# Optimization experiments

Hardware: AMD Instinct MI355X
Metric: run time of the kernel (lower is better)

## Reference

```python
import jax, jax.numpy as jnp
import numpy as np

N = 10000      # nodes
E = 160000     # edges (avg degree 16)
D = 480        # node feat dim: 128x0e+64x1e+32x2e
SH = 9         # spherical harmonics dim, lmax=2, component norm
NB = 128       # radial basis count
H = 4          # attention heads
HD = D // H    # 120 = 32x0e+16x1o+8x2e
L = 6          # transformer blocks
G = 256        # graphs in batch
MID = 480      # ffn mid dim (irreps_mlp_mid)
S = 128        # scalar (0e) channels used by the output head
FCH = 64       # radial MLP hidden (fc_neurons)
CUTOFF = 5.0
AVG_DEG = 16.0
AVG_NODES = 18.0


def _sph_l2(vec):
    # real spherical harmonics l=0,1,2 on normalized vectors, 'component' normalization
    r = jnp.linalg.norm(vec, axis=-1, keepdims=True)
    u = vec / (r + 1e-9)
    x, y, z = u[..., 0], u[..., 1], u[..., 2]
    s3, s15, s5 = jnp.sqrt(3.0), jnp.sqrt(15.0), jnp.sqrt(5.0)
    return jnp.stack([
        jnp.ones_like(x),
        s3 * x, s3 * y, s3 * z,
        s15 * x * y, s15 * y * z, 0.5 * s5 * (3.0 * z * z - 1.0),
        s15 * x * z, 0.5 * s15 * (x * x - y * y)], axis=-1)


def _rbf(d):
    centers = jnp.linspace(0.0, CUTOFF, NB)
    w = CUTOFF / NB
    return jnp.exp(-0.5 * ((d[:, None] - centers) / w) ** 2)  # [E, NB]


def _ln(x):
    mu = jnp.mean(x, axis=-1, keepdims=True)
    var = jnp.var(x, axis=-1, keepdims=True)
    return (x - mu) * jax.lax.rsqrt(var + 1e-5)


def _radial_mlp(rb, w1, w2, w3):
    h = jax.nn.silu(rb @ w1)
    h = jax.nn.silu(h @ w2)
    return h @ w3


def _segment_softmax(logits, seg, num_segments):
    m = jax.ops.segment_max(logits, seg, num_segments=num_segments)
    ex = jnp.exp(logits - m[seg])
    s = jax.ops.segment_sum(ex, seg, num_segments=num_segments)
    return ex / (s[seg] + 1e-9)


def setup_inputs():
    key = jax.random.key(0)
    ks = jax.random.split(key, 24)
    def rn(k, shape, scale):
        return jax.random.normal(k, shape, dtype=jnp.float32) * scale
    return {
        'z': jax.random.randint(ks[0], (N,), 0, 100),
        'pos': jax.random.normal(ks[1], (N, 3), dtype=jnp.float32) * 3.0,
        'batch': jnp.sort(jax.random.randint(ks[2], (N,), 0, G)),
        'edge_src': jax.random.randint(ks[3], (E,), 0, N),
        'edge_dst': jax.random.randint(ks[4], (E,), 0, N),
        'atom_emb': rn(ks[5], (100, D), 1.0),
        'W_deg_sh': rn(ks[6], (SH, D), SH ** -0.5),
        'deg_w1': rn(ks[7], (NB, FCH), NB ** -0.5),
        'deg_w2': rn(ks[8], (FCH, FCH), FCH ** -0.5),
        'deg_w3': rn(ks[9], (FCH, D), FCH ** -0.5),
        'Wv': rn(ks[10], (L, D, D), D ** -0.5),
        'Wsh': rn(ks[11], (L, SH, D), SH ** -0.5),
        'rad_w1': rn(ks[12], (L, NB, FCH), NB ** -0.5),
        'rad_w2': rn(ks[13], (L, FCH, FCH), FCH ** -0.5),
        'rad_w3': rn(ks[14], (L, FCH, D), FCH ** -0.5),
        'attn_a': rn(ks[15], (L, H, HD), HD ** -0.5),
        'Wo': rn(ks[16], (L, D, D), D ** -0.5),
        'ffn_w1': rn(ks[17], (L, D, MID), D ** -0.5),
        'ffn_w2': rn(ks[18], (L, MID, D), MID ** -0.5),
        'head_w1': rn(ks[19], (S, S), S ** -0.5),
        'head_w2': rn(ks[20], (S, S), S ** -0.5),
    }


def reference(z, pos, batch, edge_src, edge_dst, atom_emb, W_deg_sh,
              deg_w1, deg_w2, deg_w3, Wv, Wsh, rad_w1, rad_w2, rad_w3,
              attn_a, Wo, ffn_w1, ffn_w2, head_w1, head_w2):
    # edge geometry features
    vec = pos[edge_src] - pos[edge_dst]                      # [E, 3]
    sh = _sph_l2(vec)                                        # [E, SH]
    rb = _rbf(jnp.linalg.norm(vec, axis=-1))                 # [E, NB]

    # node embedding + edge-degree embedding (scatter to dst, scaled by avg degree)
    emb = atom_emb[z]                                        # [N, D]
    deg_gate = _radial_mlp(rb, deg_w1, deg_w2, deg_w3)       # [E, D]
    deg = jax.ops.segment_sum((sh @ W_deg_sh) * deg_gate, edge_dst,
                              num_segments=N) / AVG_DEG
    x = emb + deg

    # equivariant tensor-product attention blocks (gather -> per-edge TP -> segment softmax -> scatter)
    for l in range(L):
        xn = _ln(x)
        v = xn[edge_src] @ Wv[l]                             # [E, D] gather + proj
        msg = v * (sh @ Wsh[l]) * _radial_mlp(rb, rad_w1[l], rad_w2[l], rad_w3[l])
        m = msg.reshape(E, H, HD)
        logits = jnp.einsum('ehd,hd->eh', jax.nn.leaky_relu(m, 0.2), attn_a[l])
        alpha = _segment_softmax(logits, edge_dst, N)        # [E, H]
        agg = jax.ops.segment_sum(m * alpha[:, :, None], edge_dst,
                                  num_segments=N).reshape(N, D)
        x = x + agg @ Wo[l]
        x = x + jax.nn.silu(_ln(x) @ ffn_w1[l]) @ ffn_w2[l]

    # output head on scalar channels, scaled scatter over molecules
    s = _ln(x[:, :S])
    h = jax.nn.silu(s @ head_w1) @ head_w2                   # [N, S]
    out = jax.ops.segment_sum(h, batch, num_segments=G) / jnp.sqrt(AVG_NODES)
    return out
```

## Files before the change

### kernel.cpp

```cpp
#include <hip/hip_runtime.h>
#include <hip/hip_bf16.h>
#include <math.h>

#define NN 10000
#define NE 160000
#define DIM 480
#define NSH 9
#define NBASIS 128
#define NHEAD 4
#define HDIM 120
#define NL 6
#define NG 256
#define NS 128
#define FCH 64
#define CUTOFF 5.0f

typedef __attribute__((ext_vector_type(8))) short bf8v;
typedef __attribute__((ext_vector_type(4))) float f4v;

__device__ __forceinline__ float silu_f(float v) { return v / (1.0f + __expf(-v)); }
__device__ __forceinline__ float bf2f(ushort u) { return __uint_as_float(((unsigned)u) << 16); }
__device__ __forceinline__ ushort f2bfu(float f) {
  __hip_bfloat16 h = __float2bfloat16(f);
  return *reinterpret_cast<ushort*>(&h);
}

__device__ __forceinline__ void nt_store16(char* dst, uint4 v) {
  unsigned* p = (unsigned*)dst;
  __builtin_nontemporal_store(v.x, p + 0);
  __builtin_nontemporal_store(v.y, p + 1);
  __builtin_nontemporal_store(v.z, p + 2);
  __builtin_nontemporal_store(v.w, p + 3);
}
__device__ __forceinline__ uint4 nt_load16(const char* src) {
  const unsigned* p = (const unsigned*)src;
  uint4 v;
  v.x = __builtin_nontemporal_load(p + 0);
  v.y = __builtin_nontemporal_load(p + 1);
  v.z = __builtin_nontemporal_load(p + 2);
  v.w = __builtin_nontemporal_load(p + 3);
  return v;
}

struct bf16x4 { __hip_bfloat16 v[4]; };

__global__ void k_zero_int(int* p, int n)
{
  int i = blockIdx.x * 256 + threadIdx.x;
  if (i < n) p[i] = 0;
}

__global__ void k_count(const int* __restrict__ edst, int* __restrict__ cnt)
{
  int e = blockIdx.x * 256 + threadIdx.x;
  if (e < NE) atomicAdd(&cnt[edst[e]], 1);
}

__global__ __launch_bounds__(1024)
void k_scan(const int* __restrict__ cnt, int* __restrict__ row_ptr)
{
  __shared__ int part[1024];
  int tid = threadIdx.x;
  const int per = 10;
  int base = tid * per;
  int s = 0;
  for (int i = 0; i < per; i++) { int idx = base + i; if (idx < NN) s += cnt[idx]; }
  part[tid] = s; __syncthreads();
  for (int off = 1; off < 1024; off <<= 1) {
    int v = (tid >= off) ? part[tid - off] : 0;
    __syncthreads();
    part[tid] += v;
    __syncthreads();
  }
  int run = (tid > 0) ? part[tid - 1] : 0;
  for (int i = 0; i < per; i++) {
    int idx = base + i;
    if (idx < NN) { row_ptr[idx] = run; run += cnt[idx]; }
  }
  if (tid == 1023) row_ptr[NN] = part[1023];
}

__global__ void k_fill(const int* __restrict__ edst, const int* __restrict__ row_ptr,
                       int* __restrict__ cursor, int* __restrict__ csr)
{
  int e = blockIdx.x * 256 + threadIdx.x;
  if (e >= NE) return;
  int d = edst[e];
  int p = atomicAdd(&cursor[d], 1);
  csr[row_ptr[d] + p] = e;
}

__global__ void k_geom_p(const float* __restrict__ pos, const int* __restrict__ esrc,
                         const int* __restrict__ edst, const int* __restrict__ csr,
                         __hip_bfloat16* __restrict__ shb, float* __restrict__ distp,
                         int* __restrict__ esrcp, int* __restrict__ edstp)
{
  int j = blockIdx.x * 256 + threadIdx.x;
  if (j >= NE) return;
  int e = csr[j];
  int s = esrc[e], d = edst[e];
  esrcp[j] = s;
  edstp[j] = d;
  float vx = pos[s*3+0] - pos[d*3+0];
  float vy = pos[s*3+1] - pos[d*3+1];
  float vz = pos[s*3+2] - pos[d*3+2];
  float r = sqrtf(vx*vx + vy*vy + vz*vz);
  distp[j] = r;
  float inv = 1.0f / (r + 1e-9f);
  float x = vx*inv, y = vy*inv, z = vz*inv;
  const float s3 = 1.7320508075688772f;
  const float s15 = 3.872983346207417f;
  const float s5 = 2.23606797749979f;
  float sv[9];
  sv[0] = 1.0f;
  sv[1] = s3*x; sv[2] = s3*y; sv[3] = s3*z;
  sv[4] = s15*x*y; sv[5] = s15*y*z; sv[6] = 0.5f*s5*(3.0f*z*z - 1.0f);
  sv[7] = s15*x*z; sv[8] = 0.5f*s15*(x*x - y*y);
  __hip_bfloat16* o = shb + (size_t)j * 16;
#pragma unroll
  for (int q = 0; q < 9; q++) o[q] = __float2bfloat16(sv[q]);
#pragma unroll
  for (int q = 9; q < 16; q++) o[q] = __float2bfloat16(0.f);
}

__global__ void k_prep(const float* __restrict__ deg_w3, const float* __restrict__ rad_w3,
                       const float* __restrict__ W_deg_sh, const float* __restrict__ Wsh,
                       __hip_bfloat16* __restrict__ w3T, __hip_bfloat16* __restrict__ wshT)
{
  int i = blockIdx.x * 256 + threadIdx.x;
  if (i < 7*512*64) {
    int l = i / (512*64); int r = i - l*512*64; int col = r >> 6; int k = r & 63;
    float v = 0.f;
    if (col < DIM) {
      const float* src = (l == 0) ? deg_w3 : rad_w3 + (size_t)(l-1)*FCH*DIM;
      v = src[k*DIM + col];
    }
    w3T[i] = __float2bfloat16(v);
  }
  int j = i - 7*512*64;
  if (j >= 0 && j < 7*512*32) {
    int l = j / (512*32); int r = j - l*512*32; int col = r >> 5; int q = r & 31;
    float v = 0.f;
    if (col < DIM && q < 9) {
      const float* src = (l == 0) ? W_deg_sh : Wsh + (size_t)(l-1)*NSH*DIM;
      v = src[q*DIM + col];
    }
    wshT[j] = __float2bfloat16(v);
  }
}

__global__ void k_prepw(const float* __restrict__ Wv, const float* __restrict__ Wo,
                        const float* __restrict__ f1, const float* __restrict__ f2,
                        const float* __restrict__ h1, const float* __restrict__ h2w,
                        __hip_bfloat16* __restrict__ WT)
{
  int i = blockIdx.x * 256 + threadIdx.x;
  const int big = 24*512*480;
  if (i < big) {
    int m = i / (512*480); int r = i - m*(512*480); int col = r / 480; int k = r - col*480;
    int l = m % 6; int t = m / 6;
    const float* src = (t==0 ? Wv : t==1 ? Wo : t==2 ? f1 : f2) + (size_t)l*DIM*DIM;
    float v = (col < DIM) ? src[k*DIM + col] : 0.f;
    WT[i] = __float2bfloat16(v);
  } else if (i < big + 2*128*128) {
    int j = i - big; int m = j / (128*128); int r = j - m*(128*128);
    int col = r >> 7; int k = r & 127;
    const float* src = m ? h2w : h1;
    WT[i] = __float2bfloat16(src[k*128 + col]);
  }
}

__global__ __launch_bounds__(256)
void k_radial(const float* __restrict__ dist, const float* __restrict__ w1,
              const float* __restrict__ w2, __hip_bfloat16* __restrict__ h2out)
{
  __shared__ float rbs[NBASIS][65];
  __shared__ float wsm[NBASIS * FCH];
  __shared__ float ds[64];
  int tid = threadIdx.x;
  int e0 = blockIdx.x * 64;
  if (tid < 64) ds[tid] = dist[e0 + tid];
  for (int i = tid; i < NBASIS * FCH; i += 256) wsm[i] = w1[i];
  __syncthreads();
  const float invw = (float)NBASIS / CUTOFF;
  for (int i = tid; i < NBASIS * 64; i += 256) {
    int k = i >> 6, e = i & 63;
    float c = k * (CUTOFF / 127.0f);
    float tt = (ds[e] - c) * invw;
    rbs[k][e] = __expf(-0.5f * tt * tt);
  }
  __syncthreads();
  int ty = tid >> 4, tx = tid & 15;
  float acc1[4][4] = {};
  for (int k = 0; k < NBASIS; k++) {
    float b[4];
#pragma unroll
    for (int j = 0; j < 4; j++) b[j] = wsm[k*FCH + tx*4 + j];
#pragma unroll
    for (int i = 0; i < 4; i++) {
      float a = rbs[k][ty*4 + i];
#pragma unroll
      for (int j = 0; j < 4; j++) acc1[i][j] = fmaf(a, b[j], acc1[i][j]);
    }
  }
  __syncthreads();
#pragma unroll
  for (int i = 0; i < 4; i++)
#pragma unroll
    for (int j = 0; j < 4; j++)
      rbs[tx*4 + j][ty*4 + i] = silu_f(acc1[i][j]);
  for (int i = tid; i < FCH * FCH; i += 256) wsm[i] = w2[i];
  __syncthreads();
  float acc2[4][4] = {};
  for (int k = 0; k < FCH; k++) {
    float b[4];
#pragma unroll
    for (int j = 0; j < 4; j++) b[j] = wsm[k*FCH + tx*4 + j];
#pragma unroll
    for (int i = 0; i < 4; i++) {
      float a = rbs[k][ty*4 + i];
#pragma unroll
      for (int j = 0; j < 4; j++) acc2[i][j] = fmaf(a, b[j], acc2[i][j]);
    }
  }
#pragma unroll
  for (int i = 0; i < 4; i++) {
    int e = e0 + ty*4 + i;
    bf16x4 p;
#pragma unroll
    for (int j = 0; j < 4; j++) p.v[j] = __float2bfloat16(silu_f(acc2[i][j]));
    *(bf16x4*)(h2out + (size_t)e*FCH + tx*4) = p;
  }
}

__global__ __launch_bounds__(256)
void k_stats(const float* __restrict__ in, float* __restrict__ st,
             int n, int cols, int stride)
{
  int row = blockIdx.x * 4 + (threadIdx.x >> 6);
  int lane = threadIdx.x & 63;
  if (row >= n) return;
  const float* r = in + (size_t)row * stride;
  float s = 0.f, ss = 0.f;
  for (int c = lane; c < cols; c += 64) { float v = r[c]; s += v; ss += v*v; }
  for (int off = 32; off > 0; off >>= 1) { s += __shfl_down(s, off); ss += __shfl_down(ss, off); }
  if (lane == 0) {
    float mu = s / cols;
    float var = ss / cols - mu * mu;
    st[row*2]   = mu;
    st[row*2+1] = rsqrtf(fmaxf(var, 0.f) + 1e-5f);
  }
}

template<int ADD, int SILU, int LNA, int OBF16>
__global__ __launch_bounds__(256)
void k_gemmm(const float* __restrict__ A, const __hip_bfloat16* __restrict__ BT,
             float* __restrict__ C, __hip_bfloat16* __restrict__ Cb,
             const float* __restrict__ st, int M, int K, int Nc, int lda)
{
  __shared__ __align__(16) char smA[4096];
  __shared__ __align__(16) char smB[8192];
  __shared__ float smu[64], srs[64];
  int tid = threadIdx.x;
  int lane = tid & 63;
  int wv = tid >> 6;
  int l15 = lane & 15, l4 = lane >> 4;
  int row0 = blockIdx.x * 64;
  int col0 = blockIdx.y * 128;
  if (LNA && tid < 64) {
    int gr = row0 + tid;
    float m2 = 0.f, r2 = 1.f;
    if (gr < M) { m2 = st[gr*2]; r2 = st[gr*2+1]; }
    smu[tid] = m2; srs[tid] = r2;
  }
  f4v z4 = {0.f,0.f,0.f,0.f};
  f4v acc[8];
#pragma unroll
  for (int ct = 0; ct < 8; ct++) acc[ct] = z4;

  int arow = tid >> 2, aq = tid & 3;
  int bcol = tid >> 1, bh = tid & 1;
  for (int k0 = 0; k0 < K; k0 += 32) {
    __syncthreads();
    {
      int grow = row0 + arow;
      float f[8];
      if (grow < M) {
        const float* ap = A + (size_t)grow * lda + k0 + aq*8;
        float4 v0 = *(const float4*)ap;
        float4 v1 = *(const float4*)(ap + 4);
        f[0]=v0.x; f[1]=v0.y; f[2]=v0.z; f[3]=v0.w;
        f[4]=v1.x; f[5]=v1.y; f[6]=v1.z; f[7]=v1.w;
      } else {
#pragma unroll
        for (int q = 0; q < 8; q++) f[q] = 0.f;
      }
      if (LNA) {
        float mu = smu[arow], rs = srs[arow];
#pragma unroll
        for (int q = 0; q < 8; q++) f[q] = (f[q] - mu) * rs;
      }
      unsigned u[4];
#pragma unroll
      for (int q = 0; q < 4; q++)
        u[q] = (unsigned)f2bfu(f[2*q]) | ((unsigned)f2bfu(f[2*q+1]) << 16);
      int base = arow*64 + aq*16;
      *(uint4*)(smA + (base ^ ((arow&7)<<4))) = make_uint4(u[0],u[1],u[2],u[3]);
    }
    {
      const ushort* bp = (const ushort*)BT + (size_t)(col0 + bcol) * K + k0 + bh*16;
      uint4 v0 = *(const uint4*)bp;
      uint4 v1 = *(const uint4*)(bp + 8);
      int base = bcol*64 + bh*32;
      *(uint4*)(smB + (base ^ ((bcol&7)<<4))) = v0;
      *(uint4*)(smB + ((base+16) ^ ((bcol&7)<<4))) = v1;
    }
    __syncthreads();
    int r0 = wv*16 + l15;
    bf8v a0 = *(const bf8v*)(smA + ((r0*64 + l4*16) ^ ((r0&7)<<4)));
#pragma unroll
    for (int ct = 0; ct < 8; ct++) {
      int cc = ct*16 + l15;
      bf8v b = *(const bf8v*)(smB + ((cc*64 + l4*16) ^ ((cc&7)<<4)));
      acc[ct] = __builtin_amdgcn_mfma_f32_16x16x32_bf16(a0, b, acc[ct], 0, 0, 0);
    }
  }
#pragma unroll
  for (int ct = 0; ct < 8; ct++)
#pragma unroll
  for (int e = 0; e < 4; e++) {
    int row = row0 + wv*16 + l4*4 + e;
    int col = col0 + ct*16 + l15;
    if (row < M && col < Nc) {
      float v = acc[ct][e];
      if (SILU) v = silu_f(v);
      if (OBF16) Cb[(size_t)row * Nc + col] = __float2bfloat16(v);
      else {
        float* p = C + (size_t)row * Nc + col;
        if (ADD) *p += v; else *p = v;
      }
    }
  }
}

template<int MODE, int STOREM>
__global__ __launch_bounds__(256)
void k_msgm(const __hip_bfloat16* __restrict__ h2, const __hip_bfloat16* __restrict__ shb,
            const int* __restrict__ esrcp, const int* __restrict__ edstp,
            const __hip_bfloat16* __restrict__ w3T, const __hip_bfloat16* __restrict__ wshT,
            const float* __restrict__ aa, const __hip_bfloat16* __restrict__ y,
            const float* __restrict__ alpha, float* __restrict__ outbuf,
            float* __restrict__ logitsP, __hip_bfloat16* __restrict__ msgb)
{
  __shared__ __align__(16) char sm_ab[24576];
  __shared__ __align__(16) char sm_sh[4096];
  __shared__ __align__(16) char sm_wsh[8192];
  __shared__ int srcs[(MODE<=1)?64:1];
  __shared__ int dsts[(MODE>=1)?64:1];
  __shared__ int segidL[(MODE>=1)?64:1];
  __shared__ int seg_dstL[(MODE>=1)?32:1];

  int bid = blockIdx.x;
  int swzb = (bid & 7) * 1250 + (bid >> 3);
  int e0   = (swzb >> 2) * 64;
  int col0 = (swzb & 3) * 128;
  int tid = threadIdx.x;
  int lane = tid & 63;
  int wv = tid >> 6;
  int l15 = lane & 15, l4 = lane >> 4;
  int wrow0 = wv * 16;

  for (int c = tid; c < 512; c += 256) {
    int r = c >> 3, s = c & 7;
    uint4 v = *(const uint4*)((const char*)h2 + (size_t)(e0 + r) * 128 + s * 16);
    *(uint4*)(sm_ab + ((r * 128 + s * 16) ^ ((r & 7) << 4))) = v;
  }
  for (int c = tid; c < 1024; c += 256) {
    int r = c >> 3, s = c & 7;
    uint4 v = *(const uint4*)((const char*)w3T + (size_t)(col0 + r) * 128 + s * 16);
    *(uint4*)(sm_ab + 8192 + ((r * 128 + s * 16) ^ ((r & 7) << 4))) = v;
  }
  {
    int r = tid >> 2, q = tid & 3;
    uint4 v = make_uint4(0u, 0u, 0u, 0u);
    if (q < 2)
      v = *(const uint4*)((const ushort*)shb + (size_t)(e0 + r) * 16 + q * 8);
    *(uint4*)(sm_sh + ((r * 64 + q * 16) ^ ((r & 7) << 4))) = v;
  }
  for (int c = tid; c < 512; c += 256) {
    int r = c >> 2, q = c & 3;
    uint4 v = *(const uint4*)((const ushort*)wshT + (size_t)(col0 + r) * 32 + q * 8);
    *(uint4*)(sm_wsh + ((r * 64 + q * 16) ^ ((r & 7) << 4))) = v;
  }
  if (tid < 64) {
    if (MODE <= 1) srcs[tid] = esrcp[e0 + tid];
    if (MODE >= 1) dsts[tid] = edstp[e0 + tid];
  }
  __syncthreads();

  int nseg = 0;
  if (MODE >= 1) {
    if (tid < 64) {
      bool flag = (tid == 0) || (dsts[tid] != dsts[tid - 1]);
      unsigned long long m = __ballot(flag ? 1 : 0);
      unsigned long long below = m & (~0ull >> (63 - tid));
      int sg = __popcll(below) - 1;
      segidL[tid] = sg;
      if (flag && sg < 32) seg_dstL[sg] = dsts[tid];
    }
    __syncthreads();
    nseg = segidL[63] + 1;
  }

  f4v z4 = {0.f, 0.f, 0.f, 0.f};
  f4v g[8];
#pragma unroll
  for (int ct = 0; ct < 8; ct++) g[ct] = z4;

#pragma unroll
  for (int ks = 0; ks < 2; ks++) {
    int k0b = (ks * 32 + l4 * 8) * 2;
    int r0 = wrow0 + l15;
    bf8v a0 = *(const bf8v*)(sm_ab + ((r0 * 128 + k0b) ^ ((r0 & 7) << 4)));
#pragma unroll
    for (int ct = 0; ct < 8; ct++) {
      int cc = ct * 16 + l15;
      bf8v b = *(const bf8v*)(sm_ab + 8192 + ((cc * 128 + k0b) ^ ((cc & 7) << 4)));
      g[ct] = __builtin_amdgcn_mfma_f32_16x16x32_bf16(a0, b, g[ct], 0, 0, 0);
    }
  }

  const ushort* yus = (const ushort*)y;
  int srcs4[4];
  float4 al4[4];
#pragma unroll
  for (int e = 0; e < 4; e++) {
    int rl = wrow0 + l4 * 4 + e;
    if (MODE <= 1) srcs4[e] = srcs[rl];
    if (MODE == 1) al4[e] = *(const float4*)(alpha + (size_t)(e0 + rl) * 4);
  }
  {
    int r0 = wrow0 + l15;
    bf8v shA = *(const bf8v*)(sm_sh + ((r0 * 64 + l4 * 16) ^ ((r0 & 7) << 4)));
#pragma unroll
    for (int ct = 0; ct < 8; ct++) {
      int cc = ct * 16 + l15;
      int col = col0 + cc;
      bf8v wB = *(const bf8v*)(sm_wsh + ((cc * 64 + l4 * 16) ^ ((cc & 7) << 4)));
      f4v sw4 = __builtin_amdgcn_mfma_f32_16x16x32_bf16(shA, wB, z4, 0, 0, 0);
#pragma unroll
      for (int e = 0; e < 4; e++) {
        float yv;
        if (MODE == 2) yv = 1.f;
        else yv = (col < DIM) ? bf2f(yus[(size_t)srcs4[e] * DIM + col]) : 0.f;
        float mv = yv * sw4[e] * g[ct][e];
        if (MODE == 1) {
          float av = (col < 120) ? al4[e].x : (col < 240) ? al4[e].y
                   : (col < 360) ? al4[e].z : al4[e].w;
          mv *= av;
        }
        if (MODE == 2) mv *= (1.0f / 16.0f);
        g[ct][e] = mv;
      }
    }
  }

  if (MODE == 0) {
    int hA = col0 / 120;
    float aav[8];
#pragma unroll
    for (int ct = 0; ct < 8; ct++) {
      int col = col0 + ct * 16 + l15;
      aav[ct] = (col < DIM) ? aa[col] : 0.f;
    }
#pragma unroll
    for (int e = 0; e < 4; e++) {
      float sA = 0.f, sB = 0.f;
#pragma unroll
      for (int ct = 0; ct < 8; ct++) {
        int col = col0 + ct * 16 + l15;
        float mv = g[ct][e];
        float lv = (mv > 0.f) ? mv : 0.2f * mv;
        float c = lv * aav[ct];
        if (col / 120 == hA) sA += c; else sB += c;
      }
#pragma unroll
      for (int off = 1; off < 16; off <<= 1) {
        sA += __shfl_xor(sA, off, 16);
        sB += __shfl_xor(sB, off, 16);
      }
      if (l15 == 0) {
        int row = e0 + wrow0 + l4 * 4 + e;
        logitsP[((size_t)row * NHEAD + hA) * 2] = sA;
        if (hA < 3) logitsP[((size_t)row * NHEAD + hA + 1) * 2 + 1] = sB;
      }
    }
    if (STOREM) {
      __syncthreads();
#pragma unroll
      for (int ct = 0; ct < 8; ct++) {
        int cc = ct * 16 + l15;
        int ebase = wrow0 + l4 * 4;
        ushort4 pk;
        pk.x = f2bfu(g[ct][0]); pk.y = f2bfu(g[ct][1]);
        pk.z = f2bfu(g[ct][2]); pk.w = f2bfu(g[ct][3]);
        *(ushort4*)(sm_ab + ((cc * 128 + ebase * 2) ^ ((cc & 7) << 4))) = pk;
      }
      __syncthreads();
      char* gdst = (char*)msgb + (size_t)swzb * 16384;
#pragma unroll
      for (int k = 0; k < 4; k++) {
        int o = tid * 16 + k * 4096;
        uint4 v = *(const uint4*)(sm_ab + o);
        nt_store16(gdst + o, v);
      }
    }
    return;
  }

  if (nseg > 32) {
#pragma unroll
    for (int e = 0; e < 4; e++) {
      int rl = wrow0 + l4 * 4 + e;
      int dd = dsts[rl];
#pragma unroll
      for (int ct = 0; ct < 8; ct++) {
        int col = col0 + ct * 16 + l15;
        if (col < DIM) atomicAdd(&outbuf[(size_t)dd * DIM + col], g[ct][e]);
      }
    }
    return;
  }

  __syncthreads();
#pragma unroll
  for (int ct = 0; ct < 8; ct++) {
    int cc = ct * 16 + l15;
    int ebase = wrow0 + l4 * 4;
    ushort4 pk;
    pk.x = f2bfu(g[ct][0]); pk.y = f2bfu(g[ct][1]);
    pk.z = f2bfu(g[ct][2]); pk.w = f2bfu(g[ct][3]);
    *(ushort4*)(sm_ab + ((cc * 128 + ebase * 2) ^ ((cc & 7) << 4))) = pk;
  }
  __syncthreads();

  f4v p[2][2];
  p[0][0] = z4; p[0][1] = z4; p[1][0] = z4; p[1][1] = z4;
#pragma unroll
  for (int ks = 0; ks < 2; ks++) {
    int k0 = ks * 32 + l4 * 8;
    bf8v a0, a1;
#pragma unroll
    for (int e2 = 0; e2 < 8; e2++) {
      int sg = segidL[k0 + e2];
      a0[e2] = (sg == l15)      ? (short)0x3F80 : (short)0;
      a1[e2] = (sg == l15 + 16) ? (short)0x3F80 : (short)0;
    }
#pragma unroll
    for (int c2 = 0; c2 < 2; c2++) {
      int cc = (wv * 2 + c2) * 16 + l15;
      bf8v bm = *(const bf8v*)(sm_ab + ((cc * 128 + k0 * 2) ^ ((cc & 7) << 4)));
      p[0][c2] = __builtin_amdgcn_mfma_f32_16x16x32_bf16(a0, bm, p[0][c2], 0, 0, 0);
      p[1][c2] = __builtin_amdgcn_mfma_f32_16x16x32_bf16(a1, bm, p[1][c2], 0, 0, 0);
    }
  }
#pragma unroll
  for (int rt = 0; rt < 2; rt++)
#pragma unroll
  for (int c2 = 0; c2 < 2; c2++)
#pragma unroll
  for (int e = 0; e < 4; e++) {
    int seg = rt * 16 + l4 * 4 + e;
    int col = col0 + (wv * 2 + c2) * 16 + l15;
    if (seg < nseg && col < DIM) {
      float v = p[rt][c2][e];
      float* ptr = outbuf + (size_t)seg_dstL[seg] * DIM + col;
      if (seg == 0 || seg == nseg - 1) atomicAdd(ptr, v);
      else if (MODE == 1) *ptr = v;
      else *ptr += v;
    }
  }
}

__global__ __launch_bounds__(256)
void k_aggm(const __hip_bfloat16* __restrict__ msgb, const int* __restrict__ edstp,
            const float* __restrict__ alpha, float* __restrict__ agg)
{
  __shared__ __align__(16) char smM[16384];
  __shared__ __align__(16) float alsq[64][4];
  __shared__ int dsts[64];
  __shared__ int segidL[64];
  __shared__ int seg_dstL[32];

  int bid = blockIdx.x;
  int swzb = (bid & 7) * 1250 + (bid >> 3);
  int e0   = (swzb >> 2) * 64;
  int col0 = (swzb & 3) * 128;
  int tid = threadIdx.x;
  int lane = tid & 63;
  int wv = tid >> 6;
  int l15 = lane & 15, l4 = lane >> 4;

  if (tid < 64) {
    dsts[tid] = edstp[e0 + tid];
    *(float4*)&alsq[tid][0] = *(const float4*)(alpha + (size_t)(e0 + tid) * 4);
  }
  __syncthreads();

  int nseg = 0;
  if (tid < 64) {
    bool flag = (tid == 0) || (dsts[tid] != dsts[tid - 1]);
    unsigned long long m = __ballot(flag ? 1 : 0);
    unsigned long long below = m & (~0ull >> (63 - tid));
    int sg = __popcll(below) - 1;
    segidL[tid] = sg;
    if (flag && sg < 32) seg_dstL[sg] = dsts[tid];
  }
  __syncthreads();
  nseg = segidL[63] + 1;

  const char* gsrc = (const char*)msgb + (size_t)swzb * 16384;
  uint4 vv[4];
#pragma unroll
  for (int k = 0; k < 4; k++) {
    int o = tid * 16 + k * 4096;
    uint4 v = nt_load16(gsrc + o);
    int cc = o >> 7;
    int col = col0 + cc;
    int h = (col < DIM) ? (col / 120) : 3;
    int be = ((o & 127) ^ ((cc & 7) << 4)) >> 1;
    unsigned w[4] = {v.x, v.y, v.z, v.w};
#pragma unroll
    for (int q = 0; q < 4; q++) {
      float lo = bf2f((ushort)(w[q] & 0xffffu)) * alsq[be + 2*q][h];
      float hi = bf2f((ushort)(w[q] >> 16))     * alsq[be + 2*q + 1][h];
      w[q] = (unsigned)f2bfu(lo) | ((unsigned)f2bfu(hi) << 16);
    }
    vv[k] = make_uint4(w[0], w[1], w[2], w[3]);
    *(uint4*)(smM + o) = vv[k];
  }
  __syncthreads();

  if (nseg > 32) {
#pragma unroll
    for (int k = 0; k < 4; k++) {
      int o = tid * 16 + k * 4096;
      int cc = o >> 7;
      int col = col0 + cc;
      if (col >= DIM) continue;
      int be = ((o & 127) ^ ((cc & 7) << 4)) >> 1;
      unsigned w[4] = {vv[k].x, vv[k].y, vv[k].z, vv[k].w};
#pragma unroll
      for (int q = 0; q < 4; q++) {
        atomicAdd(&agg[(size_t)dsts[be + 2*q]   * DIM + col], bf2f((ushort)(w[q] & 0xffffu)));
        atomicAdd(&agg[(size_t)dsts[be + 2*q+1] * DIM + col], bf2f((ushort)(w[q] >> 16)));
      }
    }
    return;
  }

  f4v z4 = {0.f,0.f,0.f,0.f};
  f4v p[2][2];
  p[0][0] = z4; p[0][1] = z4; p[1][0] = z4; p[1][1] = z4;
#pragma unroll
  for (int ks = 0; ks < 2; ks++) {
    int k0 = ks * 32 + l4 * 8;
    bf8v a0, a1;
#pragma unroll
    for (int e2 = 0; e2 < 8; e2++) {
      int sg = segidL[k0 + e2];
      a0[e2] = (sg == l15)      ? (short)0x3F80 : (short)0;
      a1[e2] = (sg == l15 + 16) ? (short)0x3F80 : (short)0;
    }
#pragma unroll
    for (int c2 = 0; c2 < 2; c2++) {
      int cc = (wv * 2 + c2) * 16 + l15;
      bf8v bm = *(const bf8v*)(smM + ((cc * 128 + k0 * 2) ^ ((cc & 7) << 4)));
      p[0][c2] = __builtin_amdgcn_mfma_f32_16x16x32_bf16(a0, bm, p[0][c2], 0, 0, 0);
      p[1][c2] = __builtin_amdgcn_mfma_f32_16x16x32_bf16(a1, bm, p[1][c2], 0, 0, 0);
    }
  }
#pragma unroll
  for (int rt = 0; rt < 2; rt++)
#pragma unroll
  for (int c2 = 0; c2 < 2; c2++)
#pragma unroll
  for (int e = 0; e < 4; e++) {
    int seg = rt * 16 + l4 * 4 + e;
    int col = col0 + (wv * 2 + c2) * 16 + l15;
    if (seg < nseg && col < DIM) {
      float v = p[rt][c2][e];
      float* ptr = agg + (size_t)seg_dstL[seg] * DIM + col;
      if (seg == 0 || seg == nseg - 1) atomicAdd(ptr, v);
      else *ptr = v;
    }
  }
}

__global__ void k_alpha(const int* __restrict__ row_ptr, const float* __restrict__ logitsP,
                        float* __restrict__ alpha)
{
  int i = blockIdx.x * 256 + threadIdx.x;
  if (i >= NN * NHEAD) return;
  int d = i >> 2, h = i & 3;
  int beg = row_ptr[d], end = row_ptr[d+1];
  if (beg == end) return;
  float m = -1e30f;
  for (int j = beg; j < end; j++) {
    float L = logitsP[((size_t)j*NHEAD + h)*2] + logitsP[((size_t)j*NHEAD + h)*2 + 1];
    m = fmaxf(m, L);
  }
  float s = 0.f;
  for (int j = beg; j < end; j++) {
    float L = logitsP[((size_t)j*NHEAD + h)*2] + logitsP[((size_t)j*NHEAD + h)*2 + 1];
    float ex = __expf(L - m);
    alpha[(size_t)j*NHEAD + h] = ex;
    s += ex;
  }
  float inv = 1.f / (s + 1e-9f);
  for (int j = beg; j < end; j++) alpha[(size_t)j*NHEAD + h] *= inv;
}

__global__ void k_init_x(const int* __restrict__ z, const float* __restrict__ emb,
                         float* __restrict__ x)
{
  int i = blockIdx.x * 256 + threadIdx.x;
  if (i >= NN * DIM) return;
  int n = i / DIM, c = i - n * DIM;
  x[i] = emb[(size_t)z[n]*DIM + c];
}

__global__ void k_scatter(const float* __restrict__ h, const int* __restrict__ batch,
                          float* __restrict__ out)
{
  int i = blockIdx.x * 256 + threadIdx.x;
  if (i >= NN * NS) return;
  int n = i >> 7;
  atomicAdd(&out[(size_t)batch[n]*NS + (i & 127)], h[i] * 0.23570226039551584f);
}

extern "C" void kernel_launch(void* const* d_in, const int* in_sizes, int n_in,
                              void* d_out, int out_size, void* d_ws, size_t ws_size,
                              hipStream_t stream)
{
  const int*   z        = (const int*)  d_in[0];
  const float* pos      = (const float*)d_in[1];
  const int*   batch    = (const int*)  d_in[2];
  const int*   esrc     = (const int*)  d_in[3];
  const int*   edst     = (const int*)  d_in[4];
  const float* atom_emb = (const float*)d_in[5];
  const float* W_deg_sh = (const float*)d_in[6];
  const float* deg_w1   = (const float*)d_in[7];
  const float* deg_w2   = (const float*)d_in[8];
  const float* deg_w3   = (const float*)d_in[9];
  const float* Wv       = (const float*)d_in[10];
  const float* Wsh      = (const float*)d_in[11];
  const float* rad_w1   = (const float*)d_in[12];
  const float* rad_w2   = (const float*)d_in[13];
  const float* rad_w3   = (const float*)d_in[14];
  const float* attn_a   = (const float*)d_in[15];
  const float* Wo       = (const float*)d_in[16];
  const float* ffn_w1   = (const float*)d_in[17];
  const float* ffn_w2   = (const float*)d_in[18];
  const float* head_w1  = (const float*)d_in[19];
  const float* head_w2  = (const float*)d_in[20];
  float* out = (float*)d_out;

  float* x      = (float*)d_ws;
  float* statsb = x      + (size_t)NN * DIM;
  float* agg    = statsb + (size_t)NN * 2;
  float* distp  = agg    + (size_t)NN * DIM;
  float* logitsP= distp  + (size_t)NE;
  float* alphab = logitsP+ (size_t)NE * NHEAD * 2;
  __hip_bfloat16* yb    = (__hip_bfloat16*)(alphab + (size_t)NE * NHEAD);
  __hip_bfloat16* h2b   = yb + (size_t)NN * DIM;
  __hip_bfloat16* shb16 = h2b + (size_t)NE * FCH;
  __hip_bfloat16* w3Tb  = shb16 + (size_t)NE * 16;
  __hip_bfloat16* wshTb = w3Tb + (size_t)7 * 512 * 64;
  __hip_bfloat16* bigWT = wshTb + (size_t)7 * 512 * 32;
  int* cnt      = (int*)(bigWT + (size_t)24*512*480 + 2*128*128);
  int* row_ptr  = cnt + NN;
  int* csr      = row_ptr + NN + 1;
  int* cursor   = csr + NE;
  int* esrcp    = cursor + NN;
  int* edstp    = esrcp + NE;
  __hip_bfloat16* msgb = (__hip_bfloat16*)(edstp + NE);
  float* tmp = logitsP;

  size_t needed = (size_t)((char*)msgb + (size_t)10000 * 16384 - (char*)d_ws);
  bool fast = ws_size >= needed;

  dim3 b256(256);
  k_zero_int<<<(NN+255)/256, b256, 0, stream>>>(cnt, NN);
  k_count<<<(NE+255)/256, b256, 0, stream>>>(edst, cnt);
  k_scan<<<1, 1024, 0, stream>>>(cnt, row_ptr);
  k_zero_int<<<(NN+255)/256, b256, 0, stream>>>(cursor, NN);
  k_fill<<<(NE+255)/256, b256, 0, stream>>>(edst, row_ptr, cursor, csr);
  k_geom_p<<<(NE+255)/256, b256, 0, stream>>>(pos, esrc, edst, csr, shb16, distp, esrcp, edstp);
  k_prep<<<(7*512*64 + 7*512*32 + 255)/256, b256, 0, stream>>>(deg_w3, rad_w3, W_deg_sh, Wsh,
      w3Tb, wshTb);
  k_prepw<<<(24*512*480 + 2*128*128 + 255)/256, b256, 0, stream>>>(Wv, Wo, ffn_w1, ffn_w2,
      head_w1, head_w2, bigWT);
  hipMemsetAsync(logitsP, 0, (size_t)NE * NHEAD * 2 * sizeof(float), stream);

  k_radial<<<NE/64, b256, 0, stream>>>(distp, deg_w1, deg_w2, h2b);
  k_init_x<<<(NN*DIM+255)/256, b256, 0, stream>>>(z, atom_emb, x);
  k_msgm<2,0><<<10000, b256, 0, stream>>>(h2b, shb16, esrcp, edstp, w3Tb, wshTb,
      nullptr, nullptr, nullptr, x, nullptr, nullptr);

  dim3 gemm_grid(157, 4);
  dim3 head_grid(157, 1);
  for (int l = 0; l < NL; l++) {
    const float* w1_l  = rad_w1 + (size_t)l*NBASIS*FCH;
    const float* w2_l  = rad_w2 + (size_t)l*FCH*FCH;
    const float* aa_l  = attn_a + (size_t)l*NHEAD*HDIM;
    const __hip_bfloat16* w3T_l  = w3Tb  + (size_t)(l+1)*512*64;
    const __hip_bfloat16* wshT_l = wshTb + (size_t)(l+1)*512*32;
    const __hip_bfloat16* WvT_l = bigWT + (size_t)(0+l)*512*480;
    const __hip_bfloat16* WoT_l = bigWT + (size_t)(6+l)*512*480;
    const __hip_bfloat16* F1T_l = bigWT + (size_t)(12+l)*512*480;
    const __hip_bfloat16* F2T_l = bigWT + (size_t)(18+l)*512*480;

    k_stats<<<(NN+3)/4, b256, 0, stream>>>(x, statsb, NN, DIM, DIM);
    k_gemmm<0,0,1,1><<<gemm_grid, b256, 0, stream>>>(x, WvT_l, nullptr, yb, statsb,
        NN, DIM, DIM, DIM);
    k_radial<<<NE/64, b256, 0, stream>>>(distp, w1_l, w2_l, h2b);
    if (fast) {
      k_msgm<0,1><<<10000, b256, 0, stream>>>(h2b, shb16, esrcp, edstp, w3T_l, wshT_l,
          aa_l, yb, nullptr, nullptr, logitsP, msgb);
      k_alpha<<<(NN*NHEAD+255)/256, b256, 0, stream>>>(row_ptr, logitsP, alphab);
      hipMemsetAsync(agg, 0, (size_t)NN * DIM * sizeof(float), stream);
      k_aggm<<<10000, b256, 0, stream>>>(msgb, edstp, alphab, agg);
    } else {
      k_msgm<0,0><<<10000, b256, 0, stream>>>(h2b, shb16, esrcp, edstp, w3T_l, wshT_l,
          aa_l, yb, nullptr, nullptr, logitsP, nullptr);
      k_alpha<<<(NN*NHEAD+255)/256, b256, 0, stream>>>(row_ptr, logitsP, alphab);
      hipMemsetAsync(agg, 0, (size_t)NN * DIM * sizeof(float), stream);
      k_msgm<1,0><<<10000, b256, 0, stream>>>(h2b, shb16, esrcp, edstp, w3T_l, wshT_l,
          nullptr, yb, alphab, agg, nullptr, nullptr);
    }
    k_gemmm<1,0,0,0><<<gemm_grid, b256, 0, stream>>>(agg, WoT_l, x, nullptr, nullptr,
        NN, DIM, DIM, DIM);
    k_stats<<<(NN+3)/4, b256, 0, stream>>>(x, statsb, NN, DIM, DIM);
    k_gemmm<0,1,1,0><<<gemm_grid, b256, 0, stream>>>(x, F1T_l, agg, nullptr, statsb,
        NN, DIM, DIM, DIM);
    k_gemmm<1,0,0,0><<<gemm_grid, b256, 0, stream>>>(agg, F2T_l, x, nullptr, nullptr,
        NN, DIM, DIM, DIM);
  }

  const __hip_bfloat16* H1T = bigWT + (size_t)24*512*480;
  const __hip_bfloat16* H2T = H1T + 128*128;
  k_stats<<<(NN+3)/4, b256, 0, stream>>>(x, statsb, NN, NS, DIM);
  k_gemmm<0,1,1,0><<<head_grid, b256, 0, stream>>>(x, H1T, agg, nullptr, statsb,
      NN, NS, NS, DIM);
  k_gemmm<0,0,0,0><<<head_grid, b256, 0, stream>>>(agg, H2T, tmp, nullptr, nullptr,
      NN, NS, NS, NS);
  hipMemsetAsync(d_out, 0, (size_t)NG * NS * sizeof(float), stream);
  k_scatter<<<(NN*NS+255)/256, b256, 0, stream>>>(tmp, batch, out);
}
```

Baseline: 2.570 ms.

## Loop over all column tiles inside each msgm block and accumulate full logits

Each k_msgm block now handles 64 edges across all four 128-column tiles in an internal loop, instead of launching one block per (edge block, column tile). The per-edge h2 and sh tiles are loaded once and reused across tiles, and the head logits are summed in registers, so the partial-logit buffer, its memset and the two-part sum in k_alpha go away. The cost is four times fewer blocks (2500 instead of 10000) doing more serial work each, with extra syncs and per-tile weight reloads, so latency hiding may suffer.

```diff
diff --git a/kernel.cpp b/kernel.cpp
--- a/kernel.cpp
+++ b/kernel.cpp
@@ -14,6 +14,7 @@
 #define NS 128
 #define FCH 64
 #define CUTOFF 5.0f
+#define NEB 2500
 
 typedef __attribute__((ext_vector_type(8))) short bf8v;
 typedef __attribute__((ext_vector_type(4))) float f4v;
@@ -350,9 +351,10 @@
             const __hip_bfloat16* __restrict__ w3T, const __hip_bfloat16* __restrict__ wshT,
             const float* __restrict__ aa, const __hip_bfloat16* __restrict__ y,
             const float* __restrict__ alpha, float* __restrict__ outbuf,
-            float* __restrict__ logitsP, __hip_bfloat16* __restrict__ msgb)
-{
-  __shared__ __align__(16) char sm_ab[24576];
+            float* __restrict__ logits, __hip_bfloat16* __restrict__ msgb)
+{
+  __shared__ __align__(16) char sm_h2[8192];
+  __shared__ __align__(16) char sm_w3[16384];
   __shared__ __align__(16) char sm_sh[4096];
   __shared__ __align__(16) char sm_wsh[8192];
   __shared__ int srcs[(MODE<=1)?64:1];
@@ -361,9 +363,12 @@
   __shared__ int seg_dstL[(MODE>=1)?32:1];
 
   int bid = blockIdx.x;
-  int swzb = (bid & 7) * 1250 + (bid >> 3);
-  int e0   = (swzb >> 2) * 64;
-  int col0 = (swzb & 3) * 128;
+  int xcd = bid & 7;
+  const int qq = NEB >> 3, rr = NEB & 7;
+  int basee = (xcd < rr) ? xcd * (qq + 1) : rr * (qq + 1) + (xcd - rr) * qq;
+  int eblk = basee + (bid >> 3);
+  int e0 = eblk * 64;
+
   int tid = threadIdx.x;
   int lane = tid & 63;
   int wv = tid >> 6;
@@ -373,12 +378,7 @@
   for (int c = tid; c < 512; c += 256) {
     int r = c >> 3, s = c & 7;
     uint4 v = *(const uint4*)((const char*)h2 + (size_t)(e0 + r) * 128 + s * 16);
-    *(uint4*)(sm_ab + ((r * 128 + s * 16) ^ ((r & 7) << 4))) = v;
-  }
-  for (int c = tid; c < 1024; c += 256) {
-    int r = c >> 3, s = c & 7;
-    uint4 v = *(const uint4*)((const char*)w3T + (size_t)(col0 + r) * 128 + s * 16);
-    *(uint4*)(sm_ab + 8192 + ((r * 128 + s * 16) ^ ((r & 7) << 4))) = v;
+    *(uint4*)(sm_h2 + ((r * 128 + s * 16) ^ ((r & 7) << 4))) = v;
   }
   {
     int r = tid >> 2, q = tid & 3;
@@ -386,11 +386,6 @@
     if (q < 2)
       v = *(const uint4*)((const ushort*)shb + (size_t)(e0 + r) * 16 + q * 8);
     *(uint4*)(sm_sh + ((r * 64 + q * 16) ^ ((r & 7) << 4))) = v;
-  }
-  for (int c = tid; c < 512; c += 256) {
-    int r = c >> 2, q = c & 3;
-    uint4 v = *(const uint4*)((const ushort*)wshT + (size_t)(col0 + r) * 32 + q * 8);
-    *(uint4*)(sm_wsh + ((r * 64 + q * 16) ^ ((r & 7) << 4))) = v;
   }
   if (tid < 64) {
     if (MODE <= 1) srcs[tid] = esrcp[e0 + tid];
@@ -412,25 +407,6 @@
     nseg = segidL[63] + 1;
   }
 
-  f4v z4 = {0.f, 0.f, 0.f, 0.f};
-  f4v g[8];
-#pragma unroll
-  for (int ct = 0; ct < 8; ct++) g[ct] = z4;
-
-#pragma unroll
-  for (int ks = 0; ks < 2; ks++) {
-    int k0b = (ks * 32 + l4 * 8) * 2;
-    int r0 = wrow0 + l15;
-    bf8v a0 = *(const bf8v*)(sm_ab + ((r0 * 128 + k0b) ^ ((r0 & 7) << 4)));
-#pragma unroll
-    for (int ct = 0; ct < 8; ct++) {
-      int cc = ct * 16 + l15;
-      bf8v b = *(const bf8v*)(sm_ab + 8192 + ((cc * 128 + k0b) ^ ((cc & 7) << 4)));
-      g[ct] = __builtin_amdgcn_mfma_f32_16x16x32_bf16(a0, b, g[ct], 0, 0, 0);
-    }
-  }
-
-  const ushort* yus = (const ushort*)y;
   int srcs4[4];
   float4 al4[4];
 #pragma unroll
@@ -439,63 +415,134 @@
     if (MODE <= 1) srcs4[e] = srcs[rl];
     if (MODE == 1) al4[e] = *(const float4*)(alpha + (size_t)(e0 + rl) * 4);
   }
-  {
-    int r0 = wrow0 + l15;
-    bf8v shA = *(const bf8v*)(sm_sh + ((r0 * 64 + l4 * 16) ^ ((r0 & 7) << 4)));
-#pragma unroll
-    for (int ct = 0; ct < 8; ct++) {
-      int cc = ct * 16 + l15;
-      int col = col0 + cc;
-      bf8v wB = *(const bf8v*)(sm_wsh + ((cc * 64 + l4 * 16) ^ ((cc & 7) << 4)));
-      f4v sw4 = __builtin_amdgcn_mfma_f32_16x16x32_bf16(shA, wB, z4, 0, 0, 0);
-#pragma unroll
-      for (int e = 0; e < 4; e++) {
-        float yv;
-        if (MODE == 2) yv = 1.f;
-        else yv = (col < DIM) ? bf2f(yus[(size_t)srcs4[e] * DIM + col]) : 0.f;
-        float mv = yv * sw4[e] * g[ct][e];
-        if (MODE == 1) {
-          float av = (col < 120) ? al4[e].x : (col < 240) ? al4[e].y
-                   : (col < 360) ? al4[e].z : al4[e].w;
-          mv *= av;
+
+  const ushort* yus = (const ushort*)y;
+  f4v z4 = {0.f, 0.f, 0.f, 0.f};
+  float lacc[4][4];
+  if (MODE == 0) {
+#pragma unroll
+    for (int e = 0; e < 4; e++)
+#pragma unroll
+      for (int h = 0; h < 4; h++) lacc[e][h] = 0.f;
+  }
+
+#pragma unroll
+  for (int ci = 0; ci < 4; ci++) {
+    int col0 = ci * 128;
+    __syncthreads();
+    for (int c = tid; c < 1024; c += 256) {
+      int r = c >> 3, s = c & 7;
+      uint4 v = *(const uint4*)((const char*)w3T + (size_t)(col0 + r) * 128 + s * 16);
+      *(uint4*)(sm_w3 + ((r * 128 + s * 16) ^ ((r & 7) << 4))) = v;
+    }
+    for (int c = tid; c < 512; c += 256) {
+      int r = c >> 2, q = c & 3;
+      uint4 v = *(const uint4*)((const ushort*)wshT + (size_t)(col0 + r) * 32 + q * 8);
+      *(uint4*)(sm_wsh + ((r * 64 + q * 16) ^ ((r & 7) << 4))) = v;
+    }
+    __syncthreads();
+
+    f4v g[8];
+#pragma unroll
+    for (int ct = 0; ct < 8; ct++) g[ct] = z4;
+
+#pragma unroll
+    for (int ks = 0; ks < 2; ks++) {
+      int k0b = (ks * 32 + l4 * 8) * 2;
+      int r0 = wrow0 + l15;
+      bf8v a0 = *(const bf8v*)(sm_h2 + ((r0 * 128 + k0b) ^ ((r0 & 7) << 4)));
+#pragma unroll
+      for (int ct = 0; ct < 8; ct++) {
+        int cc = ct * 16 + l15;
+        bf8v b = *(const bf8v*)(sm_w3 + ((cc * 128 + k0b) ^ ((cc & 7) << 4)));
+        g[ct] = __builtin_amdgcn_mfma_f32_16x16x32_bf16(a0, b, g[ct], 0, 0, 0);
+      }
+    }
+
+    {
+      int r0 = wrow0 + l15;
+      bf8v shA = *(const bf8v*)(sm_sh + ((r0 * 64 + l4 * 16) ^ ((r0 & 7) << 4)));
+#pragma unroll
+      for (int ct = 0; ct < 8; ct++) {
+        int cc = ct * 16 + l15;
+        int col = col0 + cc;
+        bf8v wB = *(const bf8v*)(sm_wsh + ((cc * 64 + l4 * 16) ^ ((cc & 7) << 4)));
+        f4v sw4 = __builtin_amdgcn_mfma_f32_16x16x32_bf16(shA, wB, z4, 0, 0, 0);
+#pragma unroll
+        for (int e = 0; e < 4; e++) {
+          float yv;
+          if (MODE == 2) yv = 1.f;
+          else yv = (col < DIM) ? bf2f(yus[(size_t)srcs4[e] * DIM + col]) : 0.f;
+          float mv = yv * sw4[e] * g[ct][e];
+          if (MODE == 1) {
+            float av = (col < 120) ? al4[e].x : (col < 240) ? al4[e].y
+                     : (col < 360) ? al4[e].z : al4[e].w;
+            mv *= av;
+          }
+          if (MODE == 2) mv *= (1.0f / 16.0f);
+          g[ct][e] = mv;
         }
-        if (MODE == 2) mv *= (1.0f / 16.0f);
-        g[ct][e] = mv;
-      }
-    }
-  }
-
-  if (MODE == 0) {
-    int hA = col0 / 120;
-    float aav[8];
-#pragma unroll
-    for (int ct = 0; ct < 8; ct++) {
-      int col = col0 + ct * 16 + l15;
-      aav[ct] = (col < DIM) ? aa[col] : 0.f;
-    }
-#pragma unroll
-    for (int e = 0; e < 4; e++) {
-      float sA = 0.f, sB = 0.f;
+      }
+    }
+
+    if (MODE == 0) {
+      float aav[8];
 #pragma unroll
       for (int ct = 0; ct < 8; ct++) {
         int col = col0 + ct * 16 + l15;
-        float mv = g[ct][e];
-        float lv = (mv > 0.f) ? mv : 0.2f * mv;
-        float c = lv * aav[ct];
-        if (col / 120 == hA) sA += c; else sB += c;
-      }
-#pragma unroll
-      for (int off = 1; off < 16; off <<= 1) {
-        sA += __shfl_xor(sA, off, 16);
-        sB += __shfl_xor(sB, off, 16);
-      }
-      if (l15 == 0) {
-        int row = e0 + wrow0 + l4 * 4 + e;
-        logitsP[((size_t)row * NHEAD + hA) * 2] = sA;
-        if (hA < 3) logitsP[((size_t)row * NHEAD + hA + 1) * 2 + 1] = sB;
-      }
-    }
-    if (STOREM) {
+        aav[ct] = (col < DIM) ? aa[col] : 0.f;
+      }
+#pragma unroll
+      for (int e = 0; e < 4; e++) {
+        float sA = 0.f, sB = 0.f;
+#pragma unroll
+        for (int ct = 0; ct < 8; ct++) {
+          int col = col0 + ct * 16 + l15;
+          float mv = g[ct][e];
+          float lv = (mv > 0.f) ? mv : 0.2f * mv;
+          float c = lv * aav[ct];
+          if (col / 120 == ci) sA += c; else sB += c;
+        }
+#pragma unroll
+        for (int off = 1; off < 16; off <<= 1) {
+          sA += __shfl_xor(sA, off, 16);
+          sB += __shfl_xor(sB, off, 16);
+        }
+        lacc[e][ci] += sA;
+        if (ci < 3) lacc[e][ci + 1] += sB;
+      }
+      if (STOREM) {
+        __syncthreads();
+#pragma unroll
+        for (int ct = 0; ct < 8; ct++) {
+          int cc = ct * 16 + l15;
+          int ebase = wrow0 + l4 * 4;
+          ushort4 pk;
+          pk.x = f2bfu(g[ct][0]); pk.y = f2bfu(g[ct][1]);
+          pk.z = f2bfu(g[ct][2]); pk.w = f2bfu(g[ct][3]);
+          *(ushort4*)(sm_w3 + ((cc * 128 + ebase * 2) ^ ((cc & 7) << 4))) = pk;
+        }
+        __syncthreads();
+        char* gdst = (char*)msgb + (size_t)(eblk * 4 + ci) * 16384;
+#pragma unroll
+        for (int k = 0; k < 4; k++) {
+          int o = tid * 16 + k * 4096;
+          uint4 v = *(const uint4*)(sm_w3 + o);
+          nt_store16(gdst + o, v);
+        }
+      }
+    } else if (nseg > 32) {
+#pragma unroll
+      for (int e = 0; e < 4; e++) {
+        int rl = wrow0 + l4 * 4 + e;
+        int dd = dsts[rl];
+#pragma unroll
+        for (int ct = 0; ct < 8; ct++) {
+          int col = col0 + ct * 16 + l15;
+          if (col < DIM) atomicAdd(&outbuf[(size_t)dd * DIM + col], g[ct][e]);
+        }
+      }
+    } else {
       __syncthreads();
 #pragma unroll
       for (int ct = 0; ct < 8; ct++) {
@@ -504,80 +551,58 @@
         ushort4 pk;
         pk.x = f2bfu(g[ct][0]); pk.y = f2bfu(g[ct][1]);
         pk.z = f2bfu(g[ct][2]); pk.w = f2bfu(g[ct][3]);
-        *(ushort4*)(sm_ab + ((cc * 128 + ebase * 2) ^ ((cc & 7) << 4))) = pk;
+        *(ushort4*)(sm_w3 + ((cc * 128 + ebase * 2) ^ ((cc & 7) << 4))) = pk;
       }
       __syncthreads();
-      char* gdst = (char*)msgb + (size_t)swzb * 16384;
-#pragma unroll
-      for (int k = 0; k < 4; k++) {
-        int o = tid * 16 + k * 4096;
-        uint4 v = *(const uint4*)(sm_ab + o);
-        nt_store16(gdst + o, v);
-      }
-    }
-    return;
-  }
-
-  if (nseg > 32) {
+      f4v p[2][2];
+      p[0][0] = z4; p[0][1] = z4; p[1][0] = z4; p[1][1] = z4;
+#pragma unroll
+      for (int ks = 0; ks < 2; ks++) {
+        int k0 = ks * 32 + l4 * 8;
+        bf8v a0, a1;
+#pragma unroll
+        for (int e2 = 0; e2 < 8; e2++) {
+          int sg = segidL[k0 + e2];
+          a0[e2] = (sg == l15)      ? (short)0x3F80 : (short)0;
+          a1[e2] = (sg == l15 + 16) ? (short)0x3F80 : (short)0;
+        }
+#pragma unroll
+        for (int c2 = 0; c2 < 2; c2++) {
+          int cc = (wv * 2 + c2) * 16 + l15;
+          bf8v bm = *(const bf8v*)(sm_w3 + ((cc * 128 + k0 * 2) ^ ((cc & 7) << 4)));
+          p[0][c2] = __builtin_amdgcn_mfma_f32_16x16x32_bf16(a0, bm, p[0][c2], 0, 0, 0);
+          p[1][c2] = __builtin_amdgcn_mfma_f32_16x16x32_bf16(a1, bm, p[1][c2], 0, 0, 0);
+        }
+      }
+#pragma unroll
+      for (int rt = 0; rt < 2; rt++)
+#pragma unroll
+      for (int c2 = 0; c2 < 2; c2++)
+#pragma unroll
+      for (int e = 0; e < 4; e++) {
+        int seg = rt * 16 + l4 * 4 + e;
+        int col = col0 + (wv * 2 + c2) * 16 + l15;
+        if (seg < nseg && col < DIM) {
+          float v = p[rt][c2][e];
+          float* ptr = outbuf + (size_t)seg_dstL[seg] * DIM + col;
+          if (seg == 0 || seg == nseg - 1) atomicAdd(ptr, v);
+          else if (MODE == 1) *ptr = v;
+          else *ptr += v;
+        }
+      }
+    }
+  }
+
+  if (MODE == 0) {
 #pragma unroll
     for (int e = 0; e < 4; e++) {
-      int rl = wrow0 + l4 * 4 + e;
-      int dd = dsts[rl];
-#pragma unroll
-      for (int ct = 0; ct < 8; ct++) {
-        int col = col0 + ct * 16 + l15;
-        if (col < DIM) atomicAdd(&outbuf[(size_t)dd * DIM + col], g[ct][e]);
-      }
-    }
-    return;
-  }
-
-  __syncthreads();
-#pragma unroll
-  for (int ct = 0; ct < 8; ct++) {
-    int cc = ct * 16 + l15;
-    int ebase = wrow0 + l4 * 4;
-    ushort4 pk;
-    pk.x = f2bfu(g[ct][0]); pk.y = f2bfu(g[ct][1]);
-    pk.z = f2bfu(g[ct][2]); pk.w = f2bfu(g[ct][3]);
-    *(ushort4*)(sm_ab + ((cc * 128 + ebase * 2) ^ ((cc & 7) << 4))) = pk;
-  }
-  __syncthreads();
-
-  f4v p[2][2];
-  p[0][0] = z4; p[0][1] = z4; p[1][0] = z4; p[1][1] = z4;
-#pragma unroll
-  for (int ks = 0; ks < 2; ks++) {
-    int k0 = ks * 32 + l4 * 8;
-    bf8v a0, a1;
-#pragma unroll
-    for (int e2 = 0; e2 < 8; e2++) {
-      int sg = segidL[k0 + e2];
-      a0[e2] = (sg == l15)      ? (short)0x3F80 : (short)0;
-      a1[e2] = (sg == l15 + 16) ? (short)0x3F80 : (short)0;
-    }
-#pragma unroll
-    for (int c2 = 0; c2 < 2; c2++) {
-      int cc = (wv * 2 + c2) * 16 + l15;
-      bf8v bm = *(const bf8v*)(sm_ab + ((cc * 128 + k0 * 2) ^ ((cc & 7) << 4)));
-      p[0][c2] = __builtin_amdgcn_mfma_f32_16x16x32_bf16(a0, bm, p[0][c2], 0, 0, 0);
-      p[1][c2] = __builtin_amdgcn_mfma_f32_16x16x32_bf16(a1, bm, p[1][c2], 0, 0, 0);
-    }
-  }
-#pragma unroll
-  for (int rt = 0; rt < 2; rt++)
-#pragma unroll
-  for (int c2 = 0; c2 < 2; c2++)
-#pragma unroll
-  for (int e = 0; e < 4; e++) {
-    int seg = rt * 16 + l4 * 4 + e;
-    int col = col0 + (wv * 2 + c2) * 16 + l15;
-    if (seg < nseg && col < DIM) {
-      float v = p[rt][c2][e];
-      float* ptr = outbuf + (size_t)seg_dstL[seg] * DIM + col;
-      if (seg == 0 || seg == nseg - 1) atomicAdd(ptr, v);
-      else if (MODE == 1) *ptr = v;
-      else *ptr += v;
+      int row = e0 + wrow0 + l4 * 4 + e;
+      if (l15 == 0) {
+        logits[(size_t)row * 4 + 0] = lacc[e][0];
+        logits[(size_t)row * 4 + 1] = lacc[e][1];
+        logits[(size_t)row * 4 + 2] = lacc[e][2];
+        logits[(size_t)row * 4 + 3] = lacc[e][3];
+      }
     }
   }
 }
@@ -697,7 +722,7 @@
   }
 }
 
-__global__ void k_alpha(const int* __restrict__ row_ptr, const float* __restrict__ logitsP,
+__global__ void k_alpha(const int* __restrict__ row_ptr, const float* __restrict__ logits,
                         float* __restrict__ alpha)
 {
   int i = blockIdx.x * 256 + threadIdx.x;
@@ -706,14 +731,10 @@
   int beg = row_ptr[d], end = row_ptr[d+1];
   if (beg == end) return;
   float m = -1e30f;
-  for (int j = beg; j < end; j++) {
-    float L = logitsP[((size_t)j*NHEAD + h)*2] + logitsP[((size_t)j*NHEAD + h)*2 + 1];
-    m = fmaxf(m, L);
-  }
+  for (int j = beg; j < end; j++) m = fmaxf(m, logits[(size_t)j*NHEAD + h]);
   float s = 0.f;
   for (int j = beg; j < end; j++) {
-    float L = logitsP[((size_t)j*NHEAD + h)*2] + logitsP[((size_t)j*NHEAD + h)*2 + 1];
-    float ex = __expf(L - m);
+    float ex = __expf(logits[(size_t)j*NHEAD + h] - m);
     alpha[(size_t)j*NHEAD + h] = ex;
     s += ex;
   }
@@ -770,8 +791,8 @@
   float* statsb = x      + (size_t)NN * DIM;
   float* agg    = statsb + (size_t)NN * 2;
   float* distp  = agg    + (size_t)NN * DIM;
-  float* logitsP= distp  + (size_t)NE;
-  float* alphab = logitsP+ (size_t)NE * NHEAD * 2;
+  float* logitsb= distp  + (size_t)NE;
+  float* alphab = logitsb+ (size_t)NE * NHEAD * 2;
   __hip_bfloat16* yb    = (__hip_bfloat16*)(alphab + (size_t)NE * NHEAD);
   __hip_bfloat16* h2b   = yb + (size_t)NN * DIM;
   __hip_bfloat16* shb16 = h2b + (size_t)NE * FCH;
@@ -785,7 +806,7 @@
   int* esrcp    = cursor + NN;
   int* edstp    = esrcp + NE;
   __hip_bfloat16* msgb = (__hip_bfloat16*)(edstp + NE);
-  float* tmp = logitsP;
+  float* tmp = logitsb;
 
   size_t needed = (size_t)((char*)msgb + (size_t)10000 * 16384 - (char*)d_ws);
   bool fast = ws_size >= needed;
@@ -801,11 +822,10 @@
       w3Tb, wshTb);
   k_prepw<<<(24*512*480 + 2*128*128 + 255)/256, b256, 0, stream>>>(Wv, Wo, ffn_w1, ffn_w2,
       head_w1, head_w2, bigWT);
-  hipMemsetAsync(logitsP, 0, (size_t)NE * NHEAD * 2 * sizeof(float), stream);
 
   k_radial<<<NE/64, b256, 0, stream>>>(distp, deg_w1, deg_w2, h2b);
   k_init_x<<<(NN*DIM+255)/256, b256, 0, stream>>>(z, atom_emb, x);
-  k_msgm<2,0><<<10000, b256, 0, stream>>>(h2b, shb16, esrcp, edstp, w3Tb, wshTb,
+  k_msgm<2,0><<<NEB, b256, 0, stream>>>(h2b, shb16, esrcp, edstp, w3Tb, wshTb,
       nullptr, nullptr, nullptr, x, nullptr, nullptr);
 
   dim3 gemm_grid(157, 4);
@@ -826,17 +846,17 @@
         NN, DIM, DIM, DIM);
     k_radial<<<NE/64, b256, 0, stream>>>(distp, w1_l, w2_l, h2b);
     if (fast) {
-      k_msgm<0,1><<<10000, b256, 0, stream>>>(h2b, shb16, esrcp, edstp, w3T_l, wshT_l,
-          aa_l, yb, nullptr, nullptr, logitsP, msgb);
-      k_alpha<<<(NN*NHEAD+255)/256, b256, 0, stream>>>(row_ptr, logitsP, alphab);
+      k_msgm<0,1><<<NEB, b256, 0, stream>>>(h2b, shb16, esrcp, edstp, w3T_l, wshT_l,
+          aa_l, yb, nullptr, nullptr, logitsb, msgb);
+      k_alpha<<<(NN*NHEAD+255)/256, b256, 0, stream>>>(row_ptr, logitsb, alphab);
       hipMemsetAsync(agg, 0, (size_t)NN * DIM * sizeof(float), stream);
       k_aggm<<<10000, b256, 0, stream>>>(msgb, edstp, alphab, agg);
     } else {
-      k_msgm<0,0><<<10000, b256, 0, stream>>>(h2b, shb16, esrcp, edstp, w3T_l, wshT_l,
-          aa_l, yb, nullptr, nullptr, logitsP, nullptr);
-      k_alpha<<<(NN*NHEAD+255)/256, b256, 0, stream>>>(row_ptr, logitsP, alphab);
+      k_msgm<0,0><<<NEB, b256, 0, stream>>>(h2b, shb16, esrcp, edstp, w3T_l, wshT_l,
+          aa_l, yb, nullptr, nullptr, logitsb, nullptr);
+      k_alpha<<<(NN*NHEAD+255)/256, b256, 0, stream>>>(row_ptr, logitsb, alphab);
       hipMemsetAsync(agg, 0, (size_t)NN * DIM * sizeof(float), stream);
-      k_msgm<1,0><<<10000, b256, 0, stream>>>(h2b, shb16, esrcp, edstp, w3T_l, wshT_l,
+      k_msgm<1,0><<<NEB, b256, 0, stream>>>(h2b, shb16, esrcp, edstp, w3T_l, wshT_l,
           nullptr, yb, alphab, agg, nullptr, nullptr);
     }
     k_gemmm<1,0,0,0><<<gemm_grid, b256, 0, stream>>>(agg, WoT_l, x, nullptr, nullptr,
```

Measured after the change: 2.377 ms. 7.5% less time.
